# Kernel tuning notes

Measured on AMD Instinct MI355X. Metric: run time of the kernel, lower is better.

The kernel has to match this reference:

```python
import jax, jax.numpy as jnp
import numpy as np

GRID_SIZE = 5
SPLINE_ORDER = 3
GRID_LO, GRID_HI = -1.0, 1.0


def _make_grid():
    # extended knot vector: grid_size + 2*spline_order intervals
    h = (GRID_HI - GRID_LO) / GRID_SIZE
    return jnp.arange(-SPLINE_ORDER, GRID_SIZE + SPLINE_ORDER + 1, dtype=jnp.float32) * h + GRID_LO


def _b_splines(x, grid):
    # x: [N, F] -> bases [N, F, GRID_SIZE + SPLINE_ORDER] via Cox-de Boor recursion
    xg = x[..., None]
    bases = ((xg >= grid[:-1]) & (xg < grid[1:])).astype(x.dtype)
    for k in range(1, SPLINE_ORDER + 1):
        left = (xg - grid[: -(k + 1)]) / (grid[k:-1] - grid[: -(k + 1)])
        right = (grid[k + 1:] - xg) / (grid[k + 1:] - grid[1:-k])
        bases = left * bases[..., :-1] + right * bases[..., 1:]
    return bases


def _kan_linear(x, base_w, spline_w, spline_scaler, grid):
    # x: [N, in], base_w: [out, in], spline_w: [out, in, K], spline_scaler: [out, in]
    base_out = jax.nn.relu(x) @ base_w.T
    n = x.shape[0]
    sw = (spline_w * spline_scaler[..., None]).reshape(base_w.shape[0], -1)  # [out, in*K]
    spline_out = _b_splines(x, grid).reshape(n, -1) @ sw.T
    return base_out + spline_out


def _kan_conv(x, base_w, spline_w, spline_scaler, grid, k=5):
    # x: [B, C, H, W] -> KANLinear over unfolded 5x5 patches (stride 1, VALID)
    B, C, H, W = x.shape
    patches = jax.lax.conv_general_dilated_patches(x, (k, k), (1, 1), 'VALID')  # [B, C*k*k, Ho, Wo]
    Ho, Wo = patches.shape[2], patches.shape[3]
    p = patches.transpose(0, 2, 3, 1).reshape(B * Ho * Wo, C * k * k)
    out = _kan_linear(p, base_w, spline_w, spline_scaler, grid)
    return out.reshape(B, Ho, Wo, -1).transpose(0, 3, 1, 2)


def _avgpool2(x):
    B, C, H, W = x.shape
    return x.reshape(B, C, H // 2, 2, W // 2, 2).mean(axis=(3, 5))


def setup_inputs() -> dict:
    key = jax.random.key(0)
    ks = jax.random.split(key, 13)
    s = 0.1
    return {
        'x': jax.random.normal(ks[0], (1024, 1, 28, 28), jnp.float32),
        'c1_base_w': jax.random.normal(ks[1], (6, 25), jnp.float32) * s,
        'c1_spline_w': jax.random.normal(ks[2], (6, 25, 8), jnp.float32) * s,
        'c1_spline_scaler': jax.random.normal(ks[3], (6, 25), jnp.float32) * s,
        'c2_base_w': jax.random.normal(ks[4], (16, 150), jnp.float32) * s,
        'c2_spline_w': jax.random.normal(ks[5], (16, 150, 8), jnp.float32) * s,
        'c2_spline_scaler': jax.random.normal(ks[6], (16, 150), jnp.float32) * s,
        'fc1_w': jax.random.normal(ks[7], (120, 256), jnp.float32) * s,
        'fc1_b': jax.random.normal(ks[8], (120,), jnp.float32) * s,
        'fc2_w': jax.random.normal(ks[9], (84, 120), jnp.float32) * s,
        'fc2_b': jax.random.normal(ks[10], (84,), jnp.float32) * s,
        'fc3_w': jax.random.normal(ks[11], (62, 84), jnp.float32) * s,
        'fc3_b': jax.random.normal(ks[12], (62,), jnp.float32) * s,
    }


def reference(x, c1_base_w, c1_spline_w, c1_spline_scaler,
              c2_base_w, c2_spline_w, c2_spline_scaler,
              fc1_w, fc1_b, fc2_w, fc2_b, fc3_w, fc3_b):
    grid = _make_grid()
    h = _kan_conv(x, c1_base_w, c1_spline_w, c1_spline_scaler, grid)   # [B,6,24,24]
    h = _avgpool2(h)                                                    # [B,6,12,12]
    h = _kan_conv(h, c2_base_w, c2_spline_w, c2_spline_scaler, grid)   # [B,16,8,8]
    h = _avgpool2(h)                                                    # [B,16,4,4]
    h = h.reshape(h.shape[0], -1)                                       # [B,256]
    h = jax.nn.relu(h @ fc1_w.T + fc1_b)
    h = jax.nn.relu(h @ fc2_w.T + fc2_b)
    return h @ fc3_w.T + fc3_b                                          # [B,62]
```

## Files before the change

### kernel.cpp

```cpp
#include <hip/hip_runtime.h>


typedef _Float16 f16;
typedef f16 f16x8 __attribute__((ext_vector_type(8)));
typedef float f32x4 __attribute__((ext_vector_type(4)));

#define ONE_SIXTH 0.16666666666666666f

__device__ __forceinline__ void spline9(float v, float* __restrict__ f) {
    float u  = 2.5f * v + 5.5f;
    bool valid = (u >= 0.0f) && (u < 11.0f);
    float fi = floorf(u);
    int   i  = (int)fi;
    float w  = u - fi;
    float omw = 1.0f - w;
    float w2 = w * w, w3 = w2 * w;
    float c0 = omw * omw * omw * ONE_SIXTH;
    float c1 = (3.0f * w3 - 6.0f * w2 + 4.0f) * ONE_SIXTH;
    float c2 = (-3.0f * w3 + 3.0f * w2 + 3.0f * w + 1.0f) * ONE_SIXTH;
    float c3 = w3 * ONE_SIXTH;
    int j0 = i - 3;
#pragma unroll
    for (int j = 0; j < 8; ++j) {
        int d = j - j0;
        float val = (d == 0) ? c0 : (d == 1) ? c1 : (d == 2) ? c2 : (d == 3) ? c3 : 0.0f;
        f[j] = valid ? val : 0.0f;
    }
    f[8] = fmaxf(v, 0.0f);
}

__device__ __forceinline__ void spline_chunks(float v, uint4& u0, uint4& u1) {
    float f[9];
    spline9(v, f);
    union { f16 h[8]; uint4 u; } a, b;
#pragma unroll
    for (int j = 0; j < 8; ++j) a.h[j] = (f16)f[j];
    b.u.x = 0u; b.u.y = 0u; b.u.z = 0u; b.u.w = 0u;
    b.h[0] = (f16)f[8];
    u0 = a.u; u1 = b.u;
}

__global__ __launch_bounds__(256) void k_prep(
    const float* __restrict__ c1_bw, const float* __restrict__ c1_sw,
    const float* __restrict__ c1_sc,
    const float* __restrict__ c2_bw, const float* __restrict__ c2_sw,
    const float* __restrict__ c2_sc,
    f16* __restrict__ W1g, f16* __restrict__ W2g)
{
    int t = blockIdx.x * 256 + threadIdx.x;
    if (t < 9216) {
        int tap = t >> 8, r = t & 255;
        int o = r >> 4, k = r & 15;
        float val = 0.0f;
        if (o < 6 && k < 9) {
            int ey = tap / 6, ex = tap - 6 * ey;
            float s = 0.0f;
            for (int a = 0; a < 2; ++a) {
                for (int b = 0; b < 2; ++b) {
                    int dy = ey - a, dx = ex - b;
                    if (dy >= 0 && dy < 5 && dx >= 0 && dx < 5) {
                        int idx = o * 25 + dy * 5 + dx;
                        s += (k == 8) ? c1_bw[idx] : c1_sw[idx * 8 + k] * c1_sc[idx];
                    }
                }
            }
            val = 0.25f * s;
        }
        W1g[t] = (f16)val;
    }
    if (t < 55296) {
        int c = t / 9216, r = t - c * 9216;
        int tap = r >> 8, rr = r & 255;
        int o = rr >> 4, k = rr & 15;
        float val = 0.0f;
        if (k < 9) {
            int ey = tap / 6, ex = tap - 6 * ey;
            float s = 0.0f;
            for (int a = 0; a < 2; ++a) {
                for (int b = 0; b < 2; ++b) {
                    int dy = ey - a, dx = ex - b;
                    if (dy >= 0 && dy < 5 && dx >= 0 && dx < 5) {
                        int idx = o * 150 + c * 25 + dy * 5 + dx;
                        s += (k == 8) ? c2_bw[idx] : c2_sw[idx * 8 + k] * c2_sc[idx];
                    }
                }
            }
            val = 0.25f * s;
        }
        W2g[t] = (f16)val;
    }
}

__global__ __launch_bounds__(192, 3) void k_conv12(
    const float* __restrict__ x, const f16* __restrict__ W1g,
    const f16* __restrict__ W2g, float* __restrict__ h2)
{
    __shared__ uint4  feat[1728];
    __shared__ float  h1l[864];
    __shared__ float4 rbuf[2][64];

    const int img = blockIdx.x;
    const int tid = threadIdx.x;
    const int lane = tid & 63, wv = tid >> 6;
    const int ln15 = lane & 15, g = lane >> 4;
    const int gh = g & 1, gt = g >> 1;

    for (int e = tid; e < 784; e += 192) {
        uint4 u0, u1;
        spline_chunks(x[img * 784 + e], u0, u1);
        int ch = e * 2;
        int q = (ch >> 3) & 7;
        feat[ch ^ q] = u0;
        feat[(ch + 1) ^ q] = u1;
    }
    __syncthreads();

    {
        int ebase[3];
#pragma unroll
        for (int t = 0; t < 3; ++t) {
            int p = (wv * 3 + t) * 16 + ln15;
            int py = p / 12, px = p - py * 12;
            ebase[t] = py * 56 + px * 2;
        }
        const f16* bptr = W1g + (gt * 16 + ln15) * 16 + gh * 8;
        f16x8 bfrag = *(const f16x8*)bptr;
        f32x4 acc[3] = {{0,0,0,0},{0,0,0,0},{0,0,0,0}};

        for (int kc = 0; kc < 18; ++kc) {
            int tap = kc * 2 + gt;
            int ey = (tap * 171) >> 10, ex = tap - ey * 6;
            int eoff = ey * 28 + ex;
            f16x8 bcur = bfrag;
            bptr += 512;
            bfrag = *(const f16x8*)bptr;
#pragma unroll
            for (int t = 0; t < 3; ++t) {
                int ch = (ebase[t] + eoff) * 2 + gh;
                ch ^= (ch >> 3) & 7;
                f16x8 afrag = *(const f16x8*)(&feat[ch]);
                acc[t] = __builtin_amdgcn_mfma_f32_16x16x32_f16(afrag, bcur, acc[t], 0, 0, 0);
            }
        }
        if (ln15 < 6) {
#pragma unroll
            for (int t = 0; t < 3; ++t) {
                int p0 = (wv * 3 + t) * 16 + g * 4;
                *(float4*)&h1l[ln15 * 144 + p0] =
                    make_float4(acc[t][0], acc[t][1], acc[t][2], acc[t][3]);
            }
        }
    }
    __syncthreads();

    for (int e = tid; e < 864; e += 192) {
        uint4 u0, u1;
        spline_chunks(h1l[e], u0, u1);
        int ch = e * 2;
        int q = (ch >> 3) & 7;
        feat[ch ^ q] = u0;
        feat[(ch + 1) ^ q] = u1;
    }
    __syncthreads();

    {
        const int py = ln15 >> 2, px = ln15 & 3;
        const int epx = py * 24 + px * 2;
        const int kk0 = wv * 36;
        const f16* bptr = W2g + ((kk0 * 2 + gt) * 16 + ln15) * 16 + gh * 8;
        f16x8 bfrag = *(const f16x8*)bptr;
        f32x4 accA = {0, 0, 0, 0}, accB = {0, 0, 0, 0};

        for (int i = 0; i < 36; i += 2) {
#pragma unroll
            for (int s = 0; s < 2; ++s) {
                int kk = kk0 + i + s;
                int c = kk / 18, tk = kk - c * 18;
                int tap = tk * 2 + gt;
                int ey = (tap * 171) >> 10, ex = tap - ey * 6;
                f16x8 bcur = bfrag;
                bptr += 512;
                bfrag = *(const f16x8*)bptr;
                int elem = c * 144 + epx + ey * 12 + ex;
                int ch = elem * 2 + gh;
                ch ^= (ch >> 3) & 7;
                f16x8 afrag = *(const f16x8*)(&feat[ch]);
                if (s == 0)
                    accA = __builtin_amdgcn_mfma_f32_16x16x32_f16(afrag, bcur, accA, 0, 0, 0);
                else
                    accB = __builtin_amdgcn_mfma_f32_16x16x32_f16(afrag, bcur, accB, 0, 0, 0);
            }
        }
        f32x4 acc = accA + accB;

        if (wv) rbuf[wv - 1][lane] = make_float4(acc[0], acc[1], acc[2], acc[3]);
        __syncthreads();
        if (wv == 0) {
            float4 r0 = rbuf[0][lane], r1 = rbuf[1][lane];
            *(float4*)&h2[img * 256 + ln15 * 16 + g * 4] =
                make_float4(acc[0] + r0.x + r1.x, acc[1] + r0.y + r1.y,
                            acc[2] + r0.z + r1.z, acc[3] + r0.w + r1.w);
        }
    }
}

__global__ __launch_bounds__(256) void k_fc(
    const float* __restrict__ h2,
    const float* __restrict__ w1, const float* __restrict__ b1,
    const float* __restrict__ w2, const float* __restrict__ b2,
    const float* __restrict__ w3, const float* __restrict__ b3,
    float* __restrict__ out)
{
    __shared__ float xin[2][260];
    __shared__ float a1[2][120];
    __shared__ float a2[2][84];
    const int tid = threadIdx.x;
    const int r0 = blockIdx.x * 2;

    for (int i = tid; i < 512; i += 256)
        xin[i >> 8][i & 255] = h2[r0 * 256 + i];
    __syncthreads();

    if (tid < 240) {
        const int o = tid >> 1, r = tid & 1;
        const float* w = w1 + o * 256;
        float s = 0.0f;
#pragma unroll 8
        for (int k = 0; k < 64; ++k) {
            float4 wv = ((const float4*)w)[k];
            float4 xv = *(const float4*)(&xin[r][k * 4]);
            s += wv.x * xv.x + wv.y * xv.y + wv.z * xv.z + wv.w * xv.w;
        }
        a1[r][o] = fmaxf(s + b1[o], 0.0f);
    }
    __syncthreads();

    if (tid < 168) {
        const int o = tid >> 1, r = tid & 1;
        const float* w = w2 + o * 120;
        float s = 0.0f;
#pragma unroll
        for (int k = 0; k < 30; ++k) {
            float4 wv = ((const float4*)w)[k];
            float4 xv = *(const float4*)(&a1[r][k * 4]);
            s += wv.x * xv.x + wv.y * xv.y + wv.z * xv.z + wv.w * xv.w;
        }
        a2[r][o] = fmaxf(s + b2[o], 0.0f);
    }
    __syncthreads();

    if (tid < 124) {
        const int o = tid >> 1, r = tid & 1;
        const float* w = w3 + o * 84;
        float s = 0.0f;
#pragma unroll
        for (int k = 0; k < 21; ++k) {
            float4 wv = ((const float4*)w)[k];
            float4 xv = *(const float4*)(&a2[r][k * 4]);
            s += wv.x * xv.x + wv.y * xv.y + wv.z * xv.z + wv.w * xv.w;
        }
        out[(r0 + r) * 62 + o] = s + b3[o];
    }
}

extern "C" void kernel_launch(void* const* d_in, const int* in_sizes, int n_in,
                              void* d_out, int out_size, void* d_ws, size_t ws_size,
                              hipStream_t stream)
{
    (void)in_sizes; (void)n_in; (void)out_size; (void)ws_size;
    const float* x      = (const float*)d_in[0];
    const float* c1_bw  = (const float*)d_in[1];
    const float* c1_sw  = (const float*)d_in[2];
    const float* c1_sc  = (const float*)d_in[3];
    const float* c2_bw  = (const float*)d_in[4];
    const float* c2_sw  = (const float*)d_in[5];
    const float* c2_sc  = (const float*)d_in[6];
    const float* fc1_w  = (const float*)d_in[7];
    const float* fc1_b  = (const float*)d_in[8];
    const float* fc2_w  = (const float*)d_in[9];
    const float* fc2_b  = (const float*)d_in[10];
    const float* fc3_w  = (const float*)d_in[11];
    const float* fc3_b  = (const float*)d_in[12];
    float* out = (float*)d_out;

    char* wsb = (char*)d_ws;
    f16*   W1g = (f16*)(wsb);
    f16*   W2g = (f16*)(wsb + 18432);
    float* h2  = (float*)(wsb + 131072);

    hipLaunchKernelGGL(k_prep, dim3(256), dim3(256), 0, stream,
                       c1_bw, c1_sw, c1_sc, c2_bw, c2_sw, c2_sc, W1g, W2g);
    hipLaunchKernelGGL(k_conv12, dim3(1024), dim3(192), 0, stream,
                       x, W1g, W2g, h2);
    hipLaunchKernelGGL(k_fc, dim3(512), dim3(256), 0, stream,
                       h2, fc1_w, fc1_b, fc2_w, fc2_b, fc3_w, fc3_b, out);
}
```

Before: 39.84 us.

## Fuse fully connected layers into conv kernel, keep h2 in shared memory

The three fully connected layers move into the tail of the conv kernel, so each block runs the MLP for its own image from shared memory. This drops the separate k_fc launch and the global write and read of the h2 intermediate. In exchange, each block now reads the FC weights on its own (1024 blocks instead of 512, with no two-row reuse), and most threads sit idle during the FC stage of the conv kernel.

```diff
diff --git a/kernel.cpp b/kernel.cpp
--- a/kernel.cpp
+++ b/kernel.cpp
@@ -93,11 +93,18 @@
 
 __global__ __launch_bounds__(192, 3) void k_conv12(
     const float* __restrict__ x, const f16* __restrict__ W1g,
-    const f16* __restrict__ W2g, float* __restrict__ h2)
+    const f16* __restrict__ W2g,
+    const float* __restrict__ w1, const float* __restrict__ b1,
+    const float* __restrict__ w2, const float* __restrict__ b2,
+    const float* __restrict__ w3, const float* __restrict__ b3,
+    float* __restrict__ out)
 {
     __shared__ uint4  feat[1728];
     __shared__ float  h1l[864];
     __shared__ float4 rbuf[2][64];
+    __shared__ float  h2l[256];
+    __shared__ float  a1[120];
+    __shared__ float  a2[84];
 
     const int img = blockIdx.x;
     const int tid = threadIdx.x;
@@ -197,69 +204,49 @@
         __syncthreads();
         if (wv == 0) {
             float4 r0 = rbuf[0][lane], r1 = rbuf[1][lane];
-            *(float4*)&h2[img * 256 + ln15 * 16 + g * 4] =
+            *(float4*)&h2l[ln15 * 16 + g * 4] =
                 make_float4(acc[0] + r0.x + r1.x, acc[1] + r0.y + r1.y,
                             acc[2] + r0.z + r1.z, acc[3] + r0.w + r1.w);
         }
     }
-}
-
-__global__ __launch_bounds__(256) void k_fc(
-    const float* __restrict__ h2,
-    const float* __restrict__ w1, const float* __restrict__ b1,
-    const float* __restrict__ w2, const float* __restrict__ b2,
-    const float* __restrict__ w3, const float* __restrict__ b3,
-    float* __restrict__ out)
-{
-    __shared__ float xin[2][260];
-    __shared__ float a1[2][120];
-    __shared__ float a2[2][84];
-    const int tid = threadIdx.x;
-    const int r0 = blockIdx.x * 2;
-
-    for (int i = tid; i < 512; i += 256)
-        xin[i >> 8][i & 255] = h2[r0 * 256 + i];
-    __syncthreads();
-
-    if (tid < 240) {
-        const int o = tid >> 1, r = tid & 1;
-        const float* w = w1 + o * 256;
+    __syncthreads();
+
+    if (tid < 120) {
+        const float* w = w1 + tid * 256;
         float s = 0.0f;
 #pragma unroll 8
         for (int k = 0; k < 64; ++k) {
-            float4 wv = ((const float4*)w)[k];
-            float4 xv = *(const float4*)(&xin[r][k * 4]);
-            s += wv.x * xv.x + wv.y * xv.y + wv.z * xv.z + wv.w * xv.w;
-        }
-        a1[r][o] = fmaxf(s + b1[o], 0.0f);
-    }
-    __syncthreads();
-
-    if (tid < 168) {
-        const int o = tid >> 1, r = tid & 1;
-        const float* w = w2 + o * 120;
+            float4 wv4 = ((const float4*)w)[k];
+            float4 xv = *(const float4*)(&h2l[k * 4]);
+            s += wv4.x * xv.x + wv4.y * xv.y + wv4.z * xv.z + wv4.w * xv.w;
+        }
+        a1[tid] = fmaxf(s + b1[tid], 0.0f);
+    }
+    __syncthreads();
+
+    if (tid < 84) {
+        const float* w = w2 + tid * 120;
         float s = 0.0f;
 #pragma unroll
         for (int k = 0; k < 30; ++k) {
-            float4 wv = ((const float4*)w)[k];
-            float4 xv = *(const float4*)(&a1[r][k * 4]);
-            s += wv.x * xv.x + wv.y * xv.y + wv.z * xv.z + wv.w * xv.w;
-        }
-        a2[r][o] = fmaxf(s + b2[o], 0.0f);
-    }
-    __syncthreads();
-
-    if (tid < 124) {
-        const int o = tid >> 1, r = tid & 1;
-        const float* w = w3 + o * 84;
+            float4 wv4 = ((const float4*)w)[k];
+            float4 xv = *(const float4*)(&a1[k * 4]);
+            s += wv4.x * xv.x + wv4.y * xv.y + wv4.z * xv.z + wv4.w * xv.w;
+        }
+        a2[tid] = fmaxf(s + b2[tid], 0.0f);
+    }
+    __syncthreads();
+
+    if (tid < 62) {
+        const float* w = w3 + tid * 84;
         float s = 0.0f;
 #pragma unroll
         for (int k = 0; k < 21; ++k) {
-            float4 wv = ((const float4*)w)[k];
-            float4 xv = *(const float4*)(&a2[r][k * 4]);
-            s += wv.x * xv.x + wv.y * xv.y + wv.z * xv.z + wv.w * xv.w;
-        }
-        out[(r0 + r) * 62 + o] = s + b3[o];
+            float4 wv4 = ((const float4*)w)[k];
+            float4 xv = *(const float4*)(&a2[k * 4]);
+            s += wv4.x * xv.x + wv4.y * xv.y + wv4.z * xv.z + wv4.w * xv.w;
+        }
+        out[img * 62 + tid] = s + b3[tid];
     }
 }
 
@@ -284,14 +271,12 @@
     float* out = (float*)d_out;
 
     char* wsb = (char*)d_ws;
-    f16*   W1g = (f16*)(wsb);
-    f16*   W2g = (f16*)(wsb + 18432);
-    float* h2  = (float*)(wsb + 131072);
+    f16* W1g = (f16*)(wsb);
+    f16* W2g = (f16*)(wsb + 18432);
 
     hipLaunchKernelGGL(k_prep, dim3(256), dim3(256), 0, stream,
                        c1_bw, c1_sw, c1_sc, c2_bw, c2_sw, c2_sc, W1g, W2g);
     hipLaunchKernelGGL(k_conv12, dim3(1024), dim3(192), 0, stream,
-                       x, W1g, W2g, h2);
-    hipLaunchKernelGGL(k_fc, dim3(512), dim3(256), 0, stream,
-                       h2, fc1_w, fc1_b, fc2_w, fc2_b, fc3_w, fc3_b, out);
-}
+                       x, W1g, W2g,
+                       fc1_w, fc1_b, fc2_w, fc2_b, fc3_w, fc3_b, out);
+}
```

Measured after the change: 44.47 us. 1.12x slower.
